# Optimization experiments

Measured on AMD Instinct MI355X. Metric: run time of the kernel, lower is better.

## Reference

```python
import jax, jax.numpy as jnp
import numpy as np

B = 16
T_LEN, T_DIM = 149, 768
H = W = 56
S_DIM = 512
EPS = 1e-5


def setup_inputs() -> dict:
    key = jax.random.key(0)
    ks = jax.random.split(key, 12)
    N = H * W  # 3136
    return {
        "x": jax.random.normal(ks[0], (B, T_LEN, T_DIM), dtype=jnp.float32),
        "y": jax.random.normal(ks[1], (B, S_DIM, H, W), dtype=jnp.float32),
        # Conv1d(time_len -> h*w, k=1)
        "W_conv1": jax.random.normal(ks[2], (N, T_LEN), dtype=jnp.float32) * (1.0 / np.sqrt(T_LEN)),
        "b_conv1": jnp.zeros((N,), dtype=jnp.float32),
        # LayerNorms
        "ln1_g": jnp.ones((T_DIM,), dtype=jnp.float32),
        "ln1_b": jnp.zeros((T_DIM,), dtype=jnp.float32),
        "ln2_g": jnp.ones((S_DIM,), dtype=jnp.float32),
        "ln2_b": jnp.zeros((S_DIM,), dtype=jnp.float32),
        # positional encodings (1, C, H, W)
        "pe_wave": jax.random.normal(ks[3], (1, T_DIM, H, W), dtype=jnp.float32) * 0.02,
        "pe_spec": jax.random.normal(ks[4], (1, S_DIM, H, W), dtype=jnp.float32) * 0.02,
        # CrossAttention2D 1x1 convs
        "Wq": jax.random.normal(ks[5], (S_DIM, T_DIM), dtype=jnp.float32) * (1.0 / np.sqrt(T_DIM)),
        "bq": jnp.zeros((S_DIM,), dtype=jnp.float32),
        "Wk": jax.random.normal(ks[6], (S_DIM, S_DIM), dtype=jnp.float32) * (1.0 / np.sqrt(S_DIM)),
        "bk": jnp.zeros((S_DIM,), dtype=jnp.float32),
    }


def _layernorm(t, g, b):
    # t: (..., C), normalized over last axis
    m = jnp.mean(t, axis=-1, keepdims=True)
    v = jnp.mean(jnp.square(t - m), axis=-1, keepdims=True)
    return (t - m) * jax.lax.rsqrt(v + EPS) * g + b


def reference(x, y, W_conv1, b_conv1, ln1_g, ln1_b, ln2_g, ln2_b,
              pe_wave, pe_spec, Wq, bq, Wk, bk):
    # conv1d k=1 over channel dim time_len: (B,149,768) -> (B,3136,768)
    xe = jnp.einsum('bld,ol->bod', x, W_conv1) + b_conv1[None, :, None]
    # rearrange 'b (h w) c -> b h w c' (channel-last for LN/attention)
    nx = xe.reshape(x.shape[0], H, W, T_DIM)
    nx = _layernorm(nx, ln1_g, ln1_b) + pe_wave.transpose(0, 2, 3, 1)  # (B,H,W,768)

    ny = y.transpose(0, 2, 3, 1)  # (B,H,W,512)
    ny = _layernorm(ny, ln2_g, ln2_b) + pe_spec.transpose(0, 2, 3, 1)

    # 1x1 convs -> q, k; value is norm_y itself
    q = jnp.einsum('bhwc,oc->bhwo', nx, Wq) + bq  # (B,H,W,512)
    k = jnp.einsum('bhwc,oc->bhwo', ny, Wk) + bk  # (B,H,W,512)
    v = ny

    # row-local attention: each (b,h) row of W=56 tokens attends within itself
    scores = jnp.einsum('bhqc,bhkc->bhqk', q, k) / jnp.sqrt(jnp.float32(S_DIM))
    attn = jax.nn.softmax(scores, axis=-1)  # (B,H,W,W)
    out = jnp.einsum('bhqk,bhkc->bhqc', attn, v)  # (B,H,W,512)

    # permute back to (B,C,H,W), residual add
    return out.transpose(0, 3, 1, 2) + y
```

## Files before the change

kernel.cpp:

```cpp
#include <hip/hip_runtime.h>
#include <hip/hip_bf16.h>
#include <math.h>

typedef short bf16x8 __attribute__((ext_vector_type(8)));
typedef float f32x4 __attribute__((ext_vector_type(4)));

#define LN_EPS 1e-5f

static __device__ __forceinline__ float b2f(unsigned short u){
  unsigned int x = ((unsigned int)u) << 16; float f; __builtin_memcpy(&f,&x,4); return f;
}
static __device__ __forceinline__ unsigned short f2b(float f){
  unsigned int x; __builtin_memcpy(&x,&f,4);
  x += 0x7fffu + ((x>>16)&1u);
  return (unsigned short)(x>>16);
}

static __device__ __forceinline__ void gload_lds16(const void* g, void* l){
  __builtin_amdgcn_global_load_lds(
      (const __attribute__((address_space(1))) unsigned int*)g,
      (__attribute__((address_space(3))) unsigned int*)l, 16, 0, 0);
}

__global__ void pack_rowpad(const float* __restrict__ src, unsigned short* __restrict__ dst,
                            int rows, int srcK, int dstK, int rowsPad){
  int idx = blockIdx.x*256 + threadIdx.x;
  if (idx >= rowsPad*dstK) return;
  int r = idx / dstK, kk = idx - r*dstK;
  float v = (r < rows && kk < srcK) ? src[(size_t)r*srcK + kk] : 0.f;
  dst[idx] = f2b(v);
}

__global__ __launch_bounds__(256) void pack_xt(const float* __restrict__ x, unsigned short* __restrict__ xt){
  __shared__ float tile[32][33];
  int b = blockIdx.z;
  int l0 = blockIdx.y*32, d0 = blockIdx.x*32;
  int tl = threadIdx.x & 31, tw = threadIdx.x >> 5;
  for (int r=0;r<32;r+=8){
    int l = l0 + tw + r;
    tile[tw+r][tl] = (l<149) ? x[((size_t)b*149 + l)*768 + d0 + tl] : 0.f;
  }
  __syncthreads();
  for (int r=0;r<32;r+=8){
    int d = d0 + tw + r;
    int l = l0 + tl;
    if (l < 160) xt[((size_t)b*768 + d)*160 + l] = f2b(tile[tl][tw+r]);
  }
}

__global__ __launch_bounds__(256) void transpose_pe(const float* __restrict__ src, float* __restrict__ dst, int C){
  __shared__ float tile[32][33];
  int c0 = blockIdx.y*32, o0 = blockIdx.x*32;
  int tl = threadIdx.x & 31, tw = threadIdx.x >> 5;
  for (int r=0;r<32;r+=8)
    tile[tw+r][tl] = src[(size_t)(c0+tw+r)*3136 + o0 + tl];
  __syncthreads();
  for (int r=0;r<32;r+=8)
    dst[(size_t)(o0+tw+r)*C + c0 + tl] = tile[tl][tw+r];
}

#define GBM 128
#define GBN 128
#define GBK 32
__global__ __launch_bounds__(256)
void gemm_nt(const unsigned short* __restrict__ A, const unsigned short* __restrict__ Bt,
             unsigned short* __restrict__ C, const float* __restrict__ bias,
             int M, int N, int K, long long aStride, long long bStride, long long cStride,
             int swz8){
  __shared__ __align__(16) unsigned short As[GBM*GBK];
  __shared__ __align__(16) unsigned short Bs[GBN*GBK];
  int bx = blockIdx.x, by = blockIdx.y;
  if (swz8){
    int id = bx + gridDim.x*by;
    int xcd = id & 7, s = id >> 3;
    int q = s / gridDim.y;
    bx = xcd*(gridDim.x >> 3) + q;
    by = s - q*gridDim.y;
  }
  const unsigned short* Ab = A + (size_t)blockIdx.z*aStride;
  const unsigned short* Bb = Bt + (size_t)blockIdx.z*bStride;
  unsigned short* Cb = C + (size_t)blockIdx.z*cStride;
  int m0 = bx*GBM, n0 = by*GBN;
  int tid = threadIdx.x;
  int lane = tid & 63, wave = tid >> 6;
  int wm = (wave >> 1)*64, wn = (wave & 1)*64;
  f32x4 acc[4][4];
  #pragma unroll
  for (int i=0;i<4;i++)
    #pragma unroll
    for (int j=0;j<4;j++) acc[i][j]=(f32x4){0.f,0.f,0.f,0.f};
  int lr = lane & 15, lk = (lane >> 4)*8;
  for (int k0 = 0; k0 < K; k0 += GBK){
    #pragma unroll
    for (int p2=0;p2<2;p2++){
      int i = p2*256 + wave*64 + lane;
      gload_lds16(Ab + (size_t)(m0 + (i>>2))*K + k0 + (i&3)*8, As + (size_t)(p2*256 + wave*64)*8);
    }
    #pragma unroll
    for (int p2=0;p2<2;p2++){
      int i = p2*256 + wave*64 + lane;
      gload_lds16(Bb + (size_t)(n0 + (i>>2))*K + k0 + (i&3)*8, Bs + (size_t)(p2*256 + wave*64)*8);
    }
    __syncthreads();
    bf16x8 af[4], bfr[4];
    #pragma unroll
    for (int mi=0;mi<4;mi++) af[mi]  = *reinterpret_cast<const bf16x8*>(&As[(wm + mi*16 + lr)*GBK + lk]);
    #pragma unroll
    for (int nj=0;nj<4;nj++) bfr[nj] = *reinterpret_cast<const bf16x8*>(&Bs[(wn + nj*16 + lr)*GBK + lk]);
    #pragma unroll
    for (int mi=0;mi<4;mi++)
      #pragma unroll
      for (int nj=0;nj<4;nj++)
        acc[mi][nj] = __builtin_amdgcn_mfma_f32_16x16x32_bf16(af[mi], bfr[nj], acc[mi][nj], 0, 0, 0);
    __syncthreads();
  }
  int er = (lane >> 4)*4;
  #pragma unroll
  for (int mi=0;mi<4;mi++)
    #pragma unroll
    for (int nj=0;nj<4;nj++){
      int col = n0 + wn + nj*16 + lr;
      float bv = bias ? bias[col] : 0.f;
      #pragma unroll
      for (int e=0;e<4;e++){
        int row = m0 + wm + mi*16 + er + e;
        if (row < M) Cb[(size_t)row*N + col] = f2b(acc[mi][nj][e] + bv);
      }
    }
}

#define MFMA16(a,b,c) __builtin_amdgcn_mfma_f32_16x16x32_bf16(a,b,c,0,0,0)
__global__ __launch_bounds__(512)
void gemm256(const unsigned short* __restrict__ A, const unsigned short* __restrict__ Bt,
             unsigned short* __restrict__ C, const float* __restrict__ bias,
             int M, int N, int K){
  __shared__ __align__(16) unsigned short lds[65536];
  int tid = threadIdx.x;
  int lane = tid & 63, wave = tid >> 6;
  int wr = wave >> 2, wc = wave & 3;
  int lr = lane & 15, lo = lane >> 4;
  int cpx = gridDim.x >> 3;
  int id = blockIdx.x;
  int sid = (id & 7)*cpx + (id >> 3);
  int nby = N >> 8;
  int bx = sid / nby, by = sid - bx*nby;
  int m0 = bx << 8, n0 = by << 8;
  int NT = K >> 6;

  f32x4 acc[8][4];
  #pragma unroll
  for (int i=0;i<8;i++)
    #pragma unroll
    for (int j=0;j<4;j++) acc[i][j]=(f32x4){0.f,0.f,0.f,0.f};

  auto STAGE = [&](int t, int h){
    if (t >= NT) return;
    int buf = t & 1, tensor = h >> 1, half = h & 1;
    int k0 = t << 6;
    unsigned short* dstbase = lds + buf*32768 + tensor*16384;
    const unsigned short* srcT = tensor ? (Bt + (size_t)n0*K) : (A + (size_t)m0*K);
    #pragma unroll
    for (int ldi=0; ldi<2; ldi++){
      int c = half*1024 + ldi*512 + tid;
      int r = c >> 3;
      int l = (c & 7) ^ (r & 7);
      gload_lds16(srcT + (size_t)r*K + k0 + l*8,
                  dstbase + (half*1024 + ldi*512 + (wave<<6))*8);
    }
  };
  const char* ldsc = reinterpret_cast<const char*>(lds);
  int swz = lr & 7;
  auto rdA = [&](int buf, int mi, int kk)->bf16x8{
    int off = buf*65536 + (wr*128 + mi*16 + lr)*128 + (((kk*4+lo) ^ swz)*16);
    return *reinterpret_cast<const bf16x8*>(ldsc + off);
  };
  auto rdB = [&](int buf, int nj, int kk)->bf16x8{
    int off = buf*65536 + 32768 + (wc*64 + nj*16 + lr)*128 + (((kk*4+lo) ^ swz)*16);
    return *reinterpret_cast<const bf16x8*>(ldsc + off);
  };

  STAGE(0,0); STAGE(0,1); STAGE(0,2); STAGE(0,3);
  asm volatile("s_waitcnt vmcnt(0)" ::: "memory");
  __builtin_amdgcn_s_barrier();

  for (int t=0; t<NT; ++t){
    int buf = t & 1;
    STAGE(t+1,0); STAGE(t+1,1); STAGE(t+1,2); STAGE(t+1,3);
    bf16x8 bfr[4][2], af[4][2];
    #pragma unroll
    for (int nj=0;nj<4;nj++){ bfr[nj][0]=rdB(buf,nj,0); bfr[nj][1]=rdB(buf,nj,1); }
    #pragma unroll
    for (int i=0;i<4;i++){ af[i][0]=rdA(buf,i,0); af[i][1]=rdA(buf,i,1); }
    asm volatile("s_waitcnt lgkmcnt(0)" ::: "memory");
    __builtin_amdgcn_s_setprio(1);
    #pragma unroll
    for (int i=0;i<4;i++)
      #pragma unroll
      for (int nj=0;nj<4;nj++){
        acc[i][nj] = MFMA16(af[i][0], bfr[nj][0], acc[i][nj]);
        acc[i][nj] = MFMA16(af[i][1], bfr[nj][1], acc[i][nj]);
      }
    __builtin_amdgcn_s_setprio(0);
    #pragma unroll
    for (int i=0;i<4;i++){ af[i][0]=rdA(buf,4+i,0); af[i][1]=rdA(buf,4+i,1); }
    asm volatile("s_waitcnt lgkmcnt(0)" ::: "memory");
    __builtin_amdgcn_s_setprio(1);
    #pragma unroll
    for (int i=0;i<4;i++)
      #pragma unroll
      for (int nj=0;nj<4;nj++){
        acc[4+i][nj] = MFMA16(af[i][0], bfr[nj][0], acc[4+i][nj]);
        acc[4+i][nj] = MFMA16(af[i][1], bfr[nj][1], acc[4+i][nj]);
      }
    __builtin_amdgcn_s_setprio(0);
    asm volatile("s_waitcnt vmcnt(0)" ::: "memory");
    __builtin_amdgcn_s_barrier();
  }

  int er = lo*4;
  #pragma unroll
  for (int nj=0;nj<4;nj++){
    int col = n0 + wc*64 + nj*16 + lr;
    float bv = bias ? bias[col] : 0.f;
    #pragma unroll
    for (int mi=0;mi<8;mi++){
      int row = m0 + wr*128 + mi*16 + er;
      #pragma unroll
      for (int e=0;e<4;e++)
        C[(size_t)(row+e)*N + col] = f2b(acc[mi][nj][e] + bv);
    }
  }
}

__global__ __launch_bounds__(256) void ln1_kernel(unsigned short* __restrict__ xe,
    const float* __restrict__ g, const float* __restrict__ be, const float* __restrict__ pet){
  int b = blockIdx.y;
  int o0 = blockIdx.x*8;
  int t = threadIdx.x;
  int lane = t & 63, wv = t >> 6;
  __shared__ float ws1[4], ws2[4];
  __shared__ float mArr[8], rArr[8];
  float vals[8][3];
  #pragma unroll
  for (int oi=0;oi<8;oi++){
    size_t base = ((size_t)b*3136 + o0 + oi)*768;
    #pragma unroll
    for (int j=0;j<3;j++) vals[oi][j] = b2f(xe[base + t + 256*j]);
  }
  #pragma unroll
  for (int oi=0;oi<8;oi++){
    float s1=0.f, s2=0.f;
    #pragma unroll
    for (int j=0;j<3;j++){ float v=vals[oi][j]; s1+=v; s2+=v*v; }
    for (int d=32; d>0; d>>=1){ s1 += __shfl_xor(s1,d); s2 += __shfl_xor(s2,d); }
    if (lane==0){ ws1[wv]=s1; ws2[wv]=s2; }
    __syncthreads();
    if (t==0){
      float a=ws1[0]+ws1[1]+ws1[2]+ws1[3];
      float c=ws2[0]+ws2[1]+ws2[2]+ws2[3];
      float m=a*(1.f/768.f);
      float var=c*(1.f/768.f)-m*m;
      mArr[oi]=m; rArr[oi]=rsqrtf(var+LN_EPS);
    }
    __syncthreads();
  }
  #pragma unroll
  for (int oi=0;oi<8;oi++){
    size_t base = ((size_t)b*3136 + o0 + oi)*768;
    size_t pb = (size_t)(o0+oi)*768;
    float m=mArr[oi], r=rArr[oi];
    #pragma unroll
    for (int j=0;j<3;j++){
      int d = t + 256*j;
      xe[base+d] = f2b((vals[oi][j]-m)*r*g[d] + be[d] + pet[pb+d]);
    }
  }
}

__global__ __launch_bounds__(256) void ln2_kernel(const float* __restrict__ y,
    unsigned short* __restrict__ ny, unsigned short* __restrict__ nyT,
    const float* __restrict__ g, const float* __restrict__ bb, const float* __restrict__ pe){
  int b = blockIdx.y;
  int o0 = blockIdx.x*32;
  int t = threadIdx.x;
  int oi = t & 31, cg = t >> 5;
  __shared__ float red1[8][33], red2[8][33];
  __shared__ float mArr[32], rArr[32];
  __shared__ unsigned short tile[32][520];
  size_t ybase = (size_t)b*512*3136 + o0;
  float vals[64];
  float s1=0.f, s2=0.f;
  #pragma unroll
  for (int ci=0; ci<64; ci++){
    int c = cg*64 + ci;
    float v = y[ybase + (size_t)c*3136 + oi];
    vals[ci] = v;
    s1 += v; s2 += v*v;
  }
  red1[cg][oi]=s1; red2[cg][oi]=s2;
  __syncthreads();
  if (t < 32){
    float a=0.f, c2=0.f;
    #pragma unroll
    for (int kk=0;kk<8;kk++){ a+=red1[kk][t]; c2+=red2[kk][t]; }
    float m=a*(1.f/512.f);
    float var=c2*(1.f/512.f)-m*m;
    mArr[t]=m; rArr[t]=rsqrtf(var+LN_EPS);
  }
  __syncthreads();
  float m = mArr[oi], r = rArr[oi];
  #pragma unroll
  for (int ci=0; ci<64; ci++){
    int c = cg*64 + ci;
    float v = (vals[ci]-m)*r*g[c] + bb[c] + pe[(size_t)c*3136 + o0 + oi];
    tile[oi][c] = f2b(v);
  }
  __syncthreads();
  size_t nybase = ((size_t)b*3136 + o0)*512;
  for (int p = t; p < 32*64; p += 256){
    int oo = p >> 6, cp = (p & 63)*8;
    *reinterpret_cast<uint4*>(ny + nybase + (size_t)oo*512 + cp) =
        *reinterpret_cast<const uint4*>(&tile[oo][cp]);
  }
  for (int c2 = t; c2 < 512; c2 += 256){
    unsigned short row[32];
    #pragma unroll
    for (int o=0;o<32;o++) row[o] = tile[o][c2];
    size_t a = ((size_t)b*512 + c2)*3136 + o0;
    #pragma unroll
    for (int u=0;u<4;u++)
      *reinterpret_cast<uint4*>(nyT + a + u*8) = *reinterpret_cast<const uint4*>(&row[u*8]);
  }
}

__global__ __launch_bounds__(256) void attn_kernel(const unsigned short* __restrict__ q,
    const unsigned short* __restrict__ k, const unsigned short* __restrict__ vT,
    const float* __restrict__ y, float* __restrict__ outp){
  int h = blockIdx.x, b = blockIdx.y;
  int tid = threadIdx.x;
  int lane = tid & 63, w = tid >> 6;
  size_t base = (size_t)b*3136 + (size_t)h*56;
  __shared__ __align__(16) float Sf[56][60];
  __shared__ __align__(16) unsigned short Sb[64*64];
  __shared__ __align__(16) float T[4][16*68];

  f32x4 acc[4];
  #pragma unroll
  for (int mi=0;mi<4;mi++) acc[mi]=(f32x4){0.f,0.f,0.f,0.f};
  int lr = lane & 15, lo = lane >> 4;
  int lk = lo*8;
  int kr = w*16 + lr; if (kr > 55) kr = 55;
  const unsigned short* krow = k + (base + kr)*512;
  for (int k0=0;k0<512;k0+=32){
    bf16x8 kf = *reinterpret_cast<const bf16x8*>(krow + k0 + lk);
    #pragma unroll
    for (int mi=0;mi<4;mi++){
      int qr = mi*16 + lr; if (qr > 55) qr = 55;
      bf16x8 qf = *reinterpret_cast<const bf16x8*>(q + (base+qr)*512 + k0 + lk);
      acc[mi] = __builtin_amdgcn_mfma_f32_16x16x32_bf16(qf, kf, acc[mi], 0,0,0);
    }
  }

  const unsigned short* vb = vT + (size_t)b*512*3136 + (size_t)h*56;
  bf16x8 vfr[2][2][4];
  #pragma unroll
  for (int pass=0; pass<2; ++pass)
    #pragma unroll
    for (int kt=0;kt<2;++kt)
      #pragma unroll
      for (int nj=0;nj<4;++nj){
        int d = w*128 + pass*64 + nj*16 + lr;
        vfr[pass][kt][nj] = *reinterpret_cast<const bf16x8*>(vb + (size_t)d*3136 + kt*32 + lk);
      }

  const float scale = 0.04419417382415922f;
  int col = w*16 + lr;
  int er = lo*4;
  if (col < 56){
    #pragma unroll
    for (int mi=0;mi<4;mi++)
      #pragma unroll
      for (int e=0;e<4;e++){
        int row = mi*16 + er + e;
        if (row < 56) Sf[row][col] = acc[mi][e]*scale;
      }
  }
  __syncthreads();

  for (int r=0;r<14;r++){
    int i = w*14 + r;
    float xv = (lane<56) ? Sf[i][lane] : -1e30f;
    float mx = xv;
    #pragma unroll
    for (int d=32; d>0; d>>=1) mx = fmaxf(mx, __shfl_xor(mx,d));
    float ev = (lane<56) ? __expf(xv-mx) : 0.f;
    float sm = ev;
    #pragma unroll
    for (int d=32; d>0; d>>=1) sm += __shfl_xor(sm,d);
    unsigned short pv = (lane<56) ? f2b(ev/sm) : (unsigned short)0;
    int bo = i*128 + ((lane*2) ^ ((i&7)<<4));
    *reinterpret_cast<unsigned short*>(reinterpret_cast<char*>(Sb) + bo) = pv;
  }
  __syncthreads();

  float* Tw = &T[w][0];
  #pragma unroll
  for (int pass=0; pass<2; ++pass){
    int nbase = w*128 + pass*64;
    bf16x8 af[2][4];
    #pragma unroll
    for (int kt=0;kt<2;++kt)
      #pragma unroll
      for (int mi=0;mi<4;++mi){
        int row = mi*16 + lr;
        int bo = row*128 + (((kt*64) + lo*16) ^ ((row&7)<<4));
        af[kt][mi] = *reinterpret_cast<const bf16x8*>(reinterpret_cast<const char*>(Sb) + bo);
      }
    f32x4 a2[4][4];
    #pragma unroll
    for (int mi=0;mi<4;mi++)
      #pragma unroll
      for (int nj=0;nj<4;nj++) a2[mi][nj]=(f32x4){0.f,0.f,0.f,0.f};
    #pragma unroll
    for (int kt=0;kt<2;++kt)
      #pragma unroll
      for (int mi=0;mi<4;++mi)
        #pragma unroll
        for (int nj=0;nj<4;++nj)
          a2[mi][nj] = __builtin_amdgcn_mfma_f32_16x16x32_bf16(af[kt][mi], vfr[pass][kt][nj], a2[mi][nj], 0,0,0);
    #pragma unroll
    for (int nj=0;nj<4;++nj){
      asm volatile("s_waitcnt lgkmcnt(0)" ::: "memory");
      __builtin_amdgcn_sched_barrier(0);
      #pragma unroll
      for (int mi=0;mi<4;++mi)
        *reinterpret_cast<f32x4*>(&Tw[lr*68 + mi*16 + er]) = a2[mi][nj];
      asm volatile("s_waitcnt lgkmcnt(0)" ::: "memory");
      __builtin_amdgcn_sched_barrier(0);
      if (lane < 56){
        size_t gb = ((size_t)b*512 + nbase + nj*16)*3136 + (size_t)h*56 + lane;
        #pragma unroll
        for (int dd=0; dd<16; ++dd)
          outp[gb + (size_t)dd*3136] = Tw[dd*68 + lane] + y[gb + (size_t)dd*3136];
      }
    }
  }
}

extern "C" void kernel_launch(void* const* d_in, const int* in_sizes, int n_in,
                              void* d_out, int out_size, void* d_ws, size_t ws_size,
                              hipStream_t stream){
  const float* x   = (const float*)d_in[0];
  const float* y   = (const float*)d_in[1];
  const float* Wc  = (const float*)d_in[2];
  const float* g1  = (const float*)d_in[4];
  const float* be1 = (const float*)d_in[5];
  const float* g2  = (const float*)d_in[6];
  const float* be2 = (const float*)d_in[7];
  const float* peW = (const float*)d_in[8];
  const float* peS = (const float*)d_in[9];
  const float* Wq  = (const float*)d_in[10];
  const float* bq  = (const float*)d_in[11];
  const float* Wk  = (const float*)d_in[12];
  const float* bk  = (const float*)d_in[13];
  float* outp = (float*)d_out;

  char* p = (char*)d_ws;
  auto alloc = [&](size_t bytes)->char*{ char* r = p; p += (bytes + 255) & ~(size_t)255; return r; };
  unsigned short* WcB = (unsigned short*)alloc((size_t)3200*160*2);
  unsigned short* xt  = (unsigned short*)alloc((size_t)16*768*160*2);
  unsigned short* WqB = (unsigned short*)alloc((size_t)512*768*2);
  unsigned short* WkB = (unsigned short*)alloc((size_t)512*512*2);
  float* peWt = (float*)alloc((size_t)3136*768*4);
  unsigned short* xe  = (unsigned short*)alloc((size_t)16*3136*768*2);
  unsigned short* ny  = (unsigned short*)alloc((size_t)16*3136*512*2);
  unsigned short* nyT = (unsigned short*)alloc((size_t)16*512*3136*2 + 256);
  unsigned short* qb  = (unsigned short*)alloc((size_t)16*3136*512*2);
  unsigned short* kb  = (unsigned short*)alloc((size_t)16*3136*512*2);

  pack_rowpad<<<dim3((3200*160+255)/256), 256, 0, stream>>>(Wc, WcB, 3136, 149, 160, 3200);
  pack_rowpad<<<dim3((512*768+255)/256), 256, 0, stream>>>(Wq, WqB, 512, 768, 768, 512);
  pack_rowpad<<<dim3((512*512+255)/256), 256, 0, stream>>>(Wk, WkB, 512, 512, 512, 512);
  pack_xt<<<dim3(24,5,16), 256, 0, stream>>>(x, xt);
  transpose_pe<<<dim3(98,24), 256, 0, stream>>>(peW, peWt, 768);

  gemm_nt<<<dim3(25,6,16), 256, 0, stream>>>(WcB, xt, xe, nullptr, 3136, 768, 160,
                                             0LL, 768LL*160LL, 3136LL*768LL, 0);
  ln1_kernel<<<dim3(392,16), 256, 0, stream>>>(xe, g1, be1, peWt);
  ln2_kernel<<<dim3(98,16), 256, 0, stream>>>(y, ny, nyT, g2, be2, peS);
  gemm256<<<dim3(392), 512, 0, stream>>>(xe, WqB, qb, bq, 50176, 512, 768);
  gemm256<<<dim3(392), 512, 0, stream>>>(ny, WkB, kb, bk, 50176, 512, 512);
  attn_kernel<<<dim3(56,16), 256, 0, stream>>>(qb, kb, nyT, y, outp);
}
```

Measured before the change: 419.3 us.

## Transpose PV MFMA to write output directly from registers, drop LDS staging

The attention kernel's second matmul is reformulated as V^T·P^T, so each lane's accumulators already map to (channel, token) positions and can be added to y and stored to global memory without the per-warp LDS transpose buffer and its waitcnt barriers. It also splits the V fragments into four 32-channel chunks, loading the later two inside the loop to cut register pressure and overlap those loads with compute. The direct stores are scattered (16 lanes contiguous per row, rows strided by 3136), which may coalesce less well than the previous 56-lane contiguous writes.

```diff
diff --git a/kernel.cpp b/kernel.cpp
--- a/kernel.cpp
+++ b/kernel.cpp
@@ -342,7 +342,6 @@
   size_t base = (size_t)b*3136 + (size_t)h*56;
   __shared__ __align__(16) float Sf[56][60];
   __shared__ __align__(16) unsigned short Sb[64*64];
-  __shared__ __align__(16) float T[4][16*68];
 
   f32x4 acc[4];
   #pragma unroll
@@ -362,15 +361,15 @@
   }
 
   const unsigned short* vb = vT + (size_t)b*512*3136 + (size_t)h*56;
-  bf16x8 vfr[2][2][4];
-  #pragma unroll
-  for (int pass=0; pass<2; ++pass)
+  bf16x8 vfr[4][2][2];
+  #pragma unroll
+  for (int hp=0; hp<2; ++hp)
     #pragma unroll
     for (int kt=0;kt<2;++kt)
       #pragma unroll
-      for (int nj=0;nj<4;++nj){
-        int d = w*128 + pass*64 + nj*16 + lr;
-        vfr[pass][kt][nj] = *reinterpret_cast<const bf16x8*>(vb + (size_t)d*3136 + kt*32 + lk);
+      for (int mi=0;mi<2;++mi){
+        int d = w*128 + hp*32 + mi*16 + lr;
+        vfr[hp][kt][mi] = *reinterpret_cast<const bf16x8*>(vb + (size_t)d*3136 + kt*32 + lk);
       }
 
   const float scale = 0.04419417382415922f;
@@ -403,47 +402,50 @@
   }
   __syncthreads();
 
-  float* Tw = &T[w][0];
-  #pragma unroll
-  for (int pass=0; pass<2; ++pass){
-    int nbase = w*128 + pass*64;
-    bf16x8 af[2][4];
+  bf16x8 pf[2][4];
+  #pragma unroll
+  for (int kt=0;kt<2;++kt)
+    #pragma unroll
+    for (int nj=0;nj<4;++nj){
+      int row = nj*16 + lr;
+      int bo = row*128 + (((kt*64) + lo*16) ^ ((row&7)<<4));
+      pf[kt][nj] = *reinterpret_cast<const bf16x8*>(reinterpret_cast<const char*>(Sb) + bo);
+    }
+
+  #pragma unroll
+  for (int hp=0; hp<4; ++hp){
+    if (hp < 2){
+      #pragma unroll
+      for (int kt=0;kt<2;++kt)
+        #pragma unroll
+        for (int mi=0;mi<2;++mi){
+          int d = w*128 + (hp+2)*32 + mi*16 + lr;
+          vfr[hp+2][kt][mi] = *reinterpret_cast<const bf16x8*>(vb + (size_t)d*3136 + kt*32 + lk);
+        }
+    }
+    f32x4 a2[2][4];
+    #pragma unroll
+    for (int mi=0;mi<2;mi++)
+      #pragma unroll
+      for (int nj=0;nj<4;nj++) a2[mi][nj]=(f32x4){0.f,0.f,0.f,0.f};
     #pragma unroll
     for (int kt=0;kt<2;++kt)
       #pragma unroll
-      for (int mi=0;mi<4;++mi){
-        int row = mi*16 + lr;
-        int bo = row*128 + (((kt*64) + lo*16) ^ ((row&7)<<4));
-        af[kt][mi] = *reinterpret_cast<const bf16x8*>(reinterpret_cast<const char*>(Sb) + bo);
-      }
-    f32x4 a2[4][4];
-    #pragma unroll
-    for (int mi=0;mi<4;mi++)
-      #pragma unroll
-      for (int nj=0;nj<4;nj++) a2[mi][nj]=(f32x4){0.f,0.f,0.f,0.f};
-    #pragma unroll
-    for (int kt=0;kt<2;++kt)
-      #pragma unroll
-      for (int mi=0;mi<4;++mi)
+      for (int mi=0;mi<2;++mi)
         #pragma unroll
         for (int nj=0;nj<4;++nj)
-          a2[mi][nj] = __builtin_amdgcn_mfma_f32_16x16x32_bf16(af[kt][mi], vfr[pass][kt][nj], a2[mi][nj], 0,0,0);
-    #pragma unroll
-    for (int nj=0;nj<4;++nj){
-      asm volatile("s_waitcnt lgkmcnt(0)" ::: "memory");
-      __builtin_amdgcn_sched_barrier(0);
-      #pragma unroll
-      for (int mi=0;mi<4;++mi)
-        *reinterpret_cast<f32x4*>(&Tw[lr*68 + mi*16 + er]) = a2[mi][nj];
-      asm volatile("s_waitcnt lgkmcnt(0)" ::: "memory");
-      __builtin_amdgcn_sched_barrier(0);
-      if (lane < 56){
-        size_t gb = ((size_t)b*512 + nbase + nj*16)*3136 + (size_t)h*56 + lane;
+          a2[mi][nj] = __builtin_amdgcn_mfma_f32_16x16x32_bf16(vfr[hp][kt][mi], pf[kt][nj], a2[mi][nj], 0,0,0);
+    #pragma unroll
+    for (int mi=0;mi<2;++mi)
+      #pragma unroll
+      for (int e=0;e<4;++e){
+        size_t rowb = ((size_t)b*512 + w*128 + hp*32 + mi*16 + er + e)*3136 + (size_t)h*56;
         #pragma unroll
-        for (int dd=0; dd<16; ++dd)
-          outp[gb + (size_t)dd*3136] = Tw[dd*68 + lane] + y[gb + (size_t)dd*3136];
-      }
-    }
+        for (int nj=0;nj<4;++nj){
+          int r = nj*16 + lr;
+          if (r < 56) outp[rowb + r] = a2[mi][nj][e] + y[rowb + r];
+        }
+      }
   }
 }
 
```

Measured after the change: 423.2 us. Within noise of the previous version (+0.9%).
